# Kernel tuning notes

Hardware: AMD Instinct MI355X
Metric: run time of the kernel (lower is better)

The kernel has to match this reference:

```python
import jax, jax.numpy as jnp
import numpy as np

L, B, S, D, H, FF, V, P = 6, 8, 1024, 768, 12, 3072, 50257, 1024
DH = D // H
EPS = 1e-5


def setup_inputs() -> dict:
    key = jax.random.key(0)
    ks = jax.random.split(key, 12)
    std = 0.02
    return {
        "x_ids": jax.random.randint(ks[0], (B, S), 0, V),
        "calibrated_mask": jax.random.normal(ks[1], (B, S, S), jnp.float32),
        "wte": jax.random.normal(ks[2], (V, D), jnp.float32) * std,
        "wpe": jax.random.normal(ks[3], (P, D), jnp.float32) * std,
        "ln1_g": jnp.ones((L, D), jnp.float32),
        "ln1_b": jnp.zeros((L, D), jnp.float32),
        "qkv_w": jax.random.normal(ks[4], (L, D, 3 * D), jnp.float32) * std,
        "qkv_b": jnp.zeros((L, 3 * D), jnp.float32),
        "ao_w": jax.random.normal(ks[5], (L, D, D), jnp.float32) * std,
        "ao_b": jnp.zeros((L, D), jnp.float32),
        "ln2_g": jnp.ones((L, D), jnp.float32),
        "ln2_b": jnp.zeros((L, D), jnp.float32),
        "fc_w": jax.random.normal(ks[6], (L, D, FF), jnp.float32) * std,
        "fc_b": jnp.zeros((L, FF), jnp.float32),
        "op_w": jax.random.normal(ks[7], (L, FF, D), jnp.float32) * std,
        "op_b": jnp.zeros((L, D), jnp.float32),
        "lnf_g": jnp.ones((D,), jnp.float32),
        "lnf_b": jnp.zeros((D,), jnp.float32),
    }


def _ln(x, g, b):
    m = jnp.mean(x, axis=-1, keepdims=True)
    v = jnp.var(x, axis=-1, keepdims=True)
    return (x - m) * jax.lax.rsqrt(v + EPS) * g + b


def _gelu_new(x):
    c = np.sqrt(2.0 / np.pi).astype(np.float32)
    return 0.5 * x * (1.0 + jnp.tanh(c * (x + 0.044715 * x * x * x)))


def _gpt2_forward(x_ids, calibrated_mask, wte, wpe, ln1_g, ln1_b, qkv_w, qkv_b,
                  ao_w, ao_b, ln2_g, ln2_b, fc_w, fc_b, op_w, op_b, lnf_g, lnf_b):
    s = x_ids.shape[1]
    h = wte[x_ids] + wpe[:s][None, :, :]  # [B,S,D]
    causal = jnp.tril(jnp.ones((s, s), bool))
    neg = jnp.finfo(h.dtype).min
    # additive mask, broadcast over heads (unsqueeze(1).repeat over n_head)
    add_mask = calibrated_mask[:, None, :, :]  # [B,1,S,S]

    def block(hid, p):
        l1g, l1b, qw, qb, aw, ab, l2g, l2b, fw, fb, ow, ob = p
        x = _ln(hid, l1g, l1b)
        qkv = x @ qw + qb  # [B,S,3D]
        q, k, v = jnp.split(qkv, 3, axis=-1)
        q = q.reshape(q.shape[0], s, H, DH).transpose(0, 2, 1, 3)
        k = k.reshape(k.shape[0], s, H, DH).transpose(0, 2, 1, 3)
        v = v.reshape(v.shape[0], s, H, DH).transpose(0, 2, 1, 3)
        scores = jnp.einsum('bhqd,bhkd->bhqk', q, k) / jnp.sqrt(jnp.asarray(DH, q.dtype))
        scores = jnp.where(causal[None, None], scores, neg)
        scores = scores + add_mask
        w = jax.nn.softmax(scores, axis=-1)
        a = jnp.einsum('bhqk,bhkd->bhqd', w, v)
        a = a.transpose(0, 2, 1, 3).reshape(a.shape[0], s, D)
        hid = hid + a @ aw + ab
        x2 = _ln(hid, l2g, l2b)
        hid = hid + _gelu_new(x2 @ fw + fb) @ ow + ob
        return hid, None

    params = (ln1_g, ln1_b, qkv_w, qkv_b, ao_w, ao_b, ln2_g, ln2_b, fc_w, fc_b, op_w, op_b)
    h, _ = jax.lax.scan(block, h, params)
    return _ln(h, lnf_g, lnf_b)


def reference(x_ids, calibrated_mask, wte, wpe, ln1_g, ln1_b, qkv_w, qkv_b,
              ao_w, ao_b, ln2_g, ln2_b, fc_w, fc_b, op_w, op_b, lnf_g, lnf_b):
    return _gpt2_forward(x_ids, calibrated_mask, wte, wpe, ln1_g, ln1_b, qkv_w, qkv_b,
                         ao_w, ao_b, ln2_g, ln2_b, fc_w, fc_b, op_w, op_b, lnf_g, lnf_b)
```

## Files before the change

### kernel.cpp

```cpp
#include <hip/hip_runtime.h>
#include <hip/hip_bf16.h>

typedef __bf16 bf16_t;
typedef __bf16 bf16x8 __attribute__((ext_vector_type(8)));
typedef float  f32x4  __attribute__((ext_vector_type(4)));

#define DEV __device__ __forceinline__

DEV void gload_lds16(const void* g, void* l) {
  __builtin_amdgcn_global_load_lds(
      (__attribute__((address_space(1))) void*)(void*)g,
      (__attribute__((address_space(3))) void*)l, 16, 0, 0);
}

__global__ __launch_bounds__(256)
void transpose_cast(const float* __restrict__ in, bf16_t* __restrict__ out,
                    int K, int N) {
  __shared__ float tile[32][33];
  const int k0 = blockIdx.x * 32;
  const int n0 = blockIdx.y * 32;
  const int tx = threadIdx.x;
  const int ty = threadIdx.y;
#pragma unroll
  for (int i = 0; i < 32; i += 8)
    tile[ty + i][tx] = in[(long)(k0 + ty + i) * N + n0 + tx];
  __syncthreads();
#pragma unroll
  for (int i = 0; i < 32; i += 8)
    out[(long)(n0 + ty + i) * K + k0 + tx] = (bf16_t)tile[tx][ty + i];
}

__global__ __launch_bounds__(256)
void embed_kernel(const int* __restrict__ ids, const float* __restrict__ wte,
                  const float* __restrict__ wpe, float* __restrict__ h) {
  const int idx = blockIdx.x * 256 + threadIdx.x;
  const int col = idx % 768;
  const int row = idx / 768;
  const int s   = row & 1023;
  h[idx] = wte[(long)ids[row] * 768 + col] + wpe[s * 768 + col];
}

template <bool BF16OUT>
__global__ __launch_bounds__(256)
void ln_kernel(const float* __restrict__ x, const float* __restrict__ g,
               const float* __restrict__ b, bf16_t* __restrict__ ob,
               float* __restrict__ of) {
  const long row = blockIdx.x;
  const float* xr = x + row * 768;
  const int t = threadIdx.x;
  float v0 = xr[t], v1 = xr[t + 256], v2 = xr[t + 512];
  float s  = v0 + v1 + v2;
  float sq = v0 * v0 + v1 * v1 + v2 * v2;
#pragma unroll
  for (int o = 32; o; o >>= 1) { s += __shfl_down(s, o); sq += __shfl_down(sq, o); }
  __shared__ float red[8];
  const int w = t >> 6;
  if ((t & 63) == 0) { red[w] = s; red[4 + w] = sq; }
  __syncthreads();
  s  = red[0] + red[1] + red[2] + red[3];
  sq = red[4] + red[5] + red[6] + red[7];
  const float mean = s * (1.f / 768.f);
  const float rs = rsqrtf(sq * (1.f / 768.f) - mean * mean + 1e-5f);
  float vv[3] = {v0, v1, v2};
#pragma unroll
  for (int i = 0; i < 3; ++i) {
    const int col = t + i * 256;
    const float o2 = (vv[i] - mean) * rs * g[col] + b[col];
    if (BF16OUT) ob[row * 768 + col] = (bf16_t)o2;
    else         of[row * 768 + col] = o2;
  }
}

template <int EPI, int BN>
__global__ __launch_bounds__(256)
void gemm_bt(const bf16_t* __restrict__ A, const bf16_t* __restrict__ Bt,
             const float* __restrict__ bias, float* __restrict__ Cf,
             bf16_t* __restrict__ Cb, int M, int N, int K) {
  constexpr int NI = BN / 32;
  __shared__ bf16_t As[2][128 * 64];
  __shared__ bf16_t Bs[2][BN * 64];
  const int tid  = threadIdx.x;
  const int lane = tid & 63, w = tid >> 6;
  const int col = lane & 15, s16 = lane >> 4;
  const int nbn = N / BN;
  const int cpx = gridDim.x >> 3;
  const int bid = (blockIdx.x & 7) * cpx + (blockIdx.x >> 3);
  const int bm = bid / nbn, bn = bid % nbn;
  const int wr = w >> 1, wc = w & 1;

  f32x4 acc[4][NI];
#pragma unroll
  for (int i = 0; i < 4; ++i)
#pragma unroll
    for (int j = 0; j < NI; ++j) acc[i][j] = f32x4{0.f, 0.f, 0.f, 0.f};

  const long arow0 = (long)bm * 128;
  const long brow0 = (long)bn * BN;

  auto stage = [&](int buf, int k0) {
#pragma unroll
    for (int i = 0; i < 4; ++i) {
      const int c = i * 256 + tid;
      const int row = c >> 3, slot = c & 7;
      gload_lds16(A + (arow0 + row) * (long)K + k0 + ((slot ^ (row & 7)) << 3),
                  (char*)&As[buf][0] + i * 4096 + w * 1024);
    }
#pragma unroll
    for (int i = 0; i < BN / 32; ++i) {
      const int c = i * 256 + tid;
      const int row = c >> 3, slot = c & 7;
      gload_lds16(Bt + (brow0 + row) * (long)K + k0 + ((slot ^ (row & 7)) << 3),
                  (char*)&Bs[buf][0] + i * 4096 + w * 1024);
    }
  };

  const int nt = K >> 6;
  stage(0, 0);
  __syncthreads();
  int cur = 0;

  for (int t = 0; t < nt; ++t) {
    if (t + 1 < nt) stage(cur ^ 1, (t + 1) << 6);

    bf16x8 af[2][4], bfr[2][NI];
#pragma unroll
    for (int mi = 0; mi < 4; ++mi) {
      const int row = wr * 64 + mi * 16 + col;
#pragma unroll
      for (int ks = 0; ks < 2; ++ks) {
        const int slot = ks * 4 + s16;
        af[ks][mi] = *(const bf16x8*)((char*)&As[cur][0] + row * 128 +
                                      ((slot ^ (row & 7)) << 4));
      }
    }
#pragma unroll
    for (int ni = 0; ni < NI; ++ni) {
      const int row = wc * (BN / 2) + ni * 16 + col;
#pragma unroll
      for (int ks = 0; ks < 2; ++ks) {
        const int slot = ks * 4 + s16;
        bfr[ks][ni] = *(const bf16x8*)((char*)&Bs[cur][0] + row * 128 +
                                       ((slot ^ (row & 7)) << 4));
      }
    }
#pragma unroll
    for (int ks = 0; ks < 2; ++ks)
#pragma unroll
      for (int mi = 0; mi < 4; ++mi)
#pragma unroll
        for (int ni = 0; ni < NI; ++ni)
          acc[mi][ni] = __builtin_amdgcn_mfma_f32_16x16x32_bf16(
              af[ks][mi], bfr[ks][ni], acc[mi][ni], 0, 0, 0);

    __syncthreads();
    cur ^= 1;
  }

  const int colb = bn * BN + wc * (BN / 2) + col;
  const int rowb = bm * 128 + wr * 64 + (s16 << 2);
#pragma unroll
  for (int ni = 0; ni < NI; ++ni) {
    const int ccol = colb + ni * 16;
    const float bv = bias[ccol];
#pragma unroll
    for (int mi = 0; mi < 4; ++mi) {
      const int row = rowb + mi * 16;
#pragma unroll
      for (int r = 0; r < 4; ++r) {
        const float v = acc[mi][ni][r] + bv;
        const long idx = (long)(row + r) * N + ccol;
        if (EPI == 0)      Cf[idx] = v;
        else if (EPI == 1) Cf[idx] += v;
        else if (EPI == 2) Cb[idx] = (bf16_t)v;
        else {
          const float z = 0.7978845608028654f * (v + 0.044715f * v * v * v);
          Cb[idx] = (bf16_t)(v / (1.f + __expf(-2.f * z)));
        }
      }
    }
  }
}

__global__ __launch_bounds__(256)
void attn_kernel(const bf16_t* __restrict__ qkv, const float* __restrict__ mask,
                 bf16_t* __restrict__ out) {
  __shared__ bf16_t Kl[64 * 64];
  __shared__ bf16_t Vt[64 * 64];
  __shared__ bf16_t Pl[4][16 * 64];
  const int tid = threadIdx.x, lane = tid & 63, w = tid >> 6;
  const int col = lane & 15, s16 = lane >> 4, l7 = lane & 7;
  const int qp = blockIdx.x & 7;
  const int bh = blockIdx.x >> 3;
  const int b = bh / 12, h = bh % 12;
  const int sw0 = (s16 ^ l7) << 4;
  const int sw1 = ((s16 + 4) ^ l7) << 4;
  char* const plw = (char*)&Pl[w][0];

#pragma unroll 1
  for (int pass = 0; pass < 2; ++pass) {
    const int qt = pass ? (15 - qp) : qp;
    const int qrow0 = qt * 64 + w * 16;
    const long rowQ = (long)(b * 1024 + qrow0 + col) * 2304 + h * 64;
    const bf16x8 aq0 = *(const bf16x8*)&qkv[rowQ + s16 * 8];
    const bf16x8 aq1 = *(const bf16x8*)&qkv[rowQ + 32 + s16 * 8];
    const int qb = qrow0 + s16 * 4;
    const float* mrow = mask + ((long)b * 1024 + qb) * 1024;

    float m_run[4], l_run[4];
    f32x4 o_acc[4];
#pragma unroll
    for (int r = 0; r < 4; ++r) { m_run[r] = -INFINITY; l_run[r] = 0.f; }
#pragma unroll
    for (int go = 0; go < 4; ++go) o_acc[go] = f32x4{0.f, 0.f, 0.f, 0.f};

#pragma unroll 1
    for (int kt = 0; kt <= qt; ++kt) {
      const int k0 = kt * 64;
#pragma unroll
      for (int i = 0; i < 2; ++i) {
        const int c = i * 256 + tid;
        const int krow = c >> 3, slot = c & 7;
        gload_lds16(qkv + (long)(b * 1024 + k0 + krow) * 2304 + 768 + h * 64 +
                        ((slot ^ (krow & 7)) << 3),
                    (char*)Kl + i * 4096 + w * 1024);
      }
#pragma unroll
      for (int i = 0; i < 2; ++i) {
        const int c = i * 256 + tid;
        const int d = c & 63, koct = c >> 6;
        const bf16_t* vsrc = qkv + (long)(b * 1024 + k0 + koct * 8) * 2304 + 1536 + h * 64 + d;
        bf16x8 tv;
#pragma unroll
        for (int j = 0; j < 8; ++j) tv[j] = vsrc[(long)j * 2304];
        *(bf16x8*)((char*)Vt + d * 128 + ((koct ^ (d & 7)) << 4)) = tv;
      }
      float msk[4][4];
#pragma unroll
      for (int g = 0; g < 4; ++g)
#pragma unroll
        for (int r = 0; r < 4; ++r)
          msk[g][r] = mrow[(long)r * 1024 + k0 + g * 16 + col];
      __syncthreads();

      f32x4 sf[4];
#pragma unroll
      for (int g = 0; g < 4; ++g) {
        const int rbyte = (g * 16 + col) * 128;
        bf16x8 bk0 = *(const bf16x8*)((char*)Kl + rbyte + sw0);
        bf16x8 bk1 = *(const bf16x8*)((char*)Kl + rbyte + sw1);
        f32x4 z = f32x4{0.f, 0.f, 0.f, 0.f};
        z = __builtin_amdgcn_mfma_f32_16x16x32_bf16(aq0, bk0, z, 0, 0, 0);
        z = __builtin_amdgcn_mfma_f32_16x16x32_bf16(aq1, bk1, z, 0, 0, 0);
        sf[g] = z;
      }

      const bool diag = (kt == qt);
      float sv[4][4];
#pragma unroll
      for (int g = 0; g < 4; ++g)
#pragma unroll
        for (int r = 0; r < 4; ++r) {
          float s = sf[g][r] * 0.125f + msk[g][r];
          if (diag && (k0 + g * 16 + col) > (qb + r)) s = -INFINITY;
          sv[g][r] = s;
        }
#pragma unroll
      for (int r = 0; r < 4; ++r) {
        float mx = fmaxf(fmaxf(sv[0][r], sv[1][r]), fmaxf(sv[2][r], sv[3][r]));
#pragma unroll
        for (int o = 8; o; o >>= 1) mx = fmaxf(mx, __shfl_xor(mx, o));
        const float m_new = fmaxf(m_run[r], mx);
        const float f = __expf(m_run[r] - m_new);
        m_run[r] = m_new;
        float sum = 0.f;
#pragma unroll
        for (int g = 0; g < 4; ++g) {
          const float p = __expf(sv[g][r] - m_new);
          sv[g][r] = p;
          sum += p;
        }
#pragma unroll
        for (int o = 8; o; o >>= 1) sum += __shfl_xor(sum, o);
        l_run[r] = l_run[r] * f + sum;
#pragma unroll
        for (int go = 0; go < 4; ++go) o_acc[go][r] *= f;
      }

#pragma unroll
      for (int g = 0; g < 4; ++g) {
        const int ks = 2 * g + (col >> 3);
#pragma unroll
        for (int r = 0; r < 4; ++r) {
          const int qr = s16 * 4 + r;
          *(bf16_t*)(plw + qr * 128 + ((ks ^ (qr & 7)) << 4) + l7 * 2) = (bf16_t)sv[g][r];
        }
      }
      const bf16x8 pa0 = *(const bf16x8*)(plw + col * 128 + sw0);
      const bf16x8 pa1 = *(const bf16x8*)(plw + col * 128 + sw1);
#pragma unroll
      for (int go = 0; go < 4; ++go) {
        const int dbyte = (go * 16 + col) * 128;
        bf16x8 bv0 = *(const bf16x8*)((char*)Vt + dbyte + sw0);
        bf16x8 bv1 = *(const bf16x8*)((char*)Vt + dbyte + sw1);
        o_acc[go] = __builtin_amdgcn_mfma_f32_16x16x32_bf16(pa0, bv0, o_acc[go], 0, 0, 0);
        o_acc[go] = __builtin_amdgcn_mfma_f32_16x16x32_bf16(pa1, bv1, o_acc[go], 0, 0, 0);
      }
      __syncthreads();
    }

    float inv[4];
#pragma unroll
    for (int r = 0; r < 4; ++r) inv[r] = 1.f / l_run[r];
#pragma unroll
    for (int go = 0; go < 4; ++go)
#pragma unroll
      for (int r = 0; r < 4; ++r)
        out[(long)(b * 1024 + qb + r) * 768 + h * 64 + go * 16 + col] =
            (bf16_t)(o_acc[go][r] * inv[r]);
  }
}

extern "C" void kernel_launch(void* const* d_in, const int* in_sizes, int n_in,
                              void* d_out, int out_size, void* d_ws, size_t ws_size,
                              hipStream_t stream) {
  const int*   x_ids = (const int*)d_in[0];
  const float* mask  = (const float*)d_in[1];
  const float* wte   = (const float*)d_in[2];
  const float* wpe   = (const float*)d_in[3];
  const float* ln1_g = (const float*)d_in[4];
  const float* ln1_b = (const float*)d_in[5];
  const float* qkv_w = (const float*)d_in[6];
  const float* qkv_b = (const float*)d_in[7];
  const float* ao_w  = (const float*)d_in[8];
  const float* ao_b  = (const float*)d_in[9];
  const float* ln2_g = (const float*)d_in[10];
  const float* ln2_b = (const float*)d_in[11];
  const float* fc_w  = (const float*)d_in[12];
  const float* fc_b  = (const float*)d_in[13];
  const float* op_w  = (const float*)d_in[14];
  const float* op_b  = (const float*)d_in[15];
  const float* lnf_g = (const float*)d_in[16];
  const float* lnf_b = (const float*)d_in[17];

  char* ws = (char*)d_ws;
  size_t off = 0;
  auto alloc = [&](size_t bytes) {
    char* p = ws + off;
    off += (bytes + 255) & ~(size_t)255;
    return p;
  };
  bf16_t* wqT = (bf16_t*)alloc(6ull * 2304 * 768 * 2);
  bf16_t* waT = (bf16_t*)alloc(6ull * 768 * 768 * 2);
  bf16_t* wfT = (bf16_t*)alloc(6ull * 3072 * 768 * 2);
  bf16_t* woT = (bf16_t*)alloc(6ull * 768 * 3072 * 2);
  float*  h   = (float*) alloc(8192ull * 768 * 4);
  bf16_t* xb  = (bf16_t*)alloc(8192ull * 768 * 2);
  bf16_t* qkv = (bf16_t*)alloc(8192ull * 2304 * 2);
  bf16_t* abf = (bf16_t*)alloc(8192ull * 768 * 2);
  bf16_t* fb  = (bf16_t*)alloc(8192ull * 3072 * 2);
  if (off > ws_size) return;

  const dim3 tb(32, 8);
  for (int l = 0; l < 6; ++l) {
    transpose_cast<<<dim3(768 / 32, 2304 / 32), tb, 0, stream>>>(
        qkv_w + (long)l * 768 * 2304, wqT + (long)l * 2304 * 768, 768, 2304);
    transpose_cast<<<dim3(768 / 32, 768 / 32), tb, 0, stream>>>(
        ao_w + (long)l * 768 * 768, waT + (long)l * 768 * 768, 768, 768);
    transpose_cast<<<dim3(768 / 32, 3072 / 32), tb, 0, stream>>>(
        fc_w + (long)l * 768 * 3072, wfT + (long)l * 3072 * 768, 768, 3072);
    transpose_cast<<<dim3(3072 / 32, 768 / 32), tb, 0, stream>>>(
        op_w + (long)l * 3072 * 768, woT + (long)l * 768 * 3072, 3072, 768);
  }

  embed_kernel<<<24576, 256, 0, stream>>>(x_ids, wte, wpe, h);

  for (int l = 0; l < 6; ++l) {
    ln_kernel<true><<<8192, 256, 0, stream>>>(h, ln1_g + l * 768, ln1_b + l * 768, xb, nullptr);
    gemm_bt<2, 128><<<64 * 18, 256, 0, stream>>>(xb, wqT + (long)l * 2304 * 768,
                                                 qkv_b + l * 2304, nullptr, qkv, 8192, 2304, 768);
    attn_kernel<<<768, 256, 0, stream>>>(qkv, mask, abf);
    gemm_bt<1, 64><<<64 * 12, 256, 0, stream>>>(abf, waT + (long)l * 768 * 768,
                                                ao_b + l * 768, h, nullptr, 8192, 768, 768);
    ln_kernel<true><<<8192, 256, 0, stream>>>(h, ln2_g + l * 768, ln2_b + l * 768, xb, nullptr);
    gemm_bt<3, 128><<<64 * 24, 256, 0, stream>>>(xb, wfT + (long)l * 3072 * 768,
                                                 fc_b + l * 3072, nullptr, fb, 8192, 3072, 768);
    gemm_bt<1, 64><<<64 * 12, 256, 0, stream>>>(fb, woT + (long)l * 768 * 3072,
                                                op_b + l * 768, h, nullptr, 8192, 768, 3072);
  }

  ln_kernel<false><<<8192, 256, 0, stream>>>(h, lnf_g, lnf_b, nullptr, (float*)d_out);
}
```

Before: 1.789 ms.

## Double-buffer K/V tiles and prefetch mask in attention kernel

The attention kernel now keeps two LDS buffers for K and transposed V. It issues the global loads for the next key tile (K via direct-to-LDS, V and mask into registers) before computing the current tile, so memory latency overlaps with the MFMA and softmax work and one barrier per iteration is removed. It also raises wave priority around the MFMA sections and adds an occupancy hint to launch bounds. The cost is double the K/V LDS footprint and more live registers for the prefetched V and mask, which could reduce occupancy.

```diff
diff --git a/kernel.cpp b/kernel.cpp
--- a/kernel.cpp
+++ b/kernel.cpp
@@ -181,11 +181,11 @@
   }
 }
 
-__global__ __launch_bounds__(256)
+__global__ __launch_bounds__(256, 3)
 void attn_kernel(const bf16_t* __restrict__ qkv, const float* __restrict__ mask,
                  bf16_t* __restrict__ out) {
-  __shared__ bf16_t Kl[64 * 64];
-  __shared__ bf16_t Vt[64 * 64];
+  __shared__ bf16_t Kl[2][64 * 64];
+  __shared__ bf16_t Vt[2][64 * 64];
   __shared__ bf16_t Pl[4][16 * 64];
   const int tid = threadIdx.x, lane = tid & 63, w = tid >> 6;
   const int col = lane & 15, s16 = lane >> 4, l7 = lane & 7;
@@ -195,6 +195,40 @@
   const int sw0 = (s16 ^ l7) << 4;
   const int sw1 = ((s16 + 4) ^ l7) << 4;
   char* const plw = (char*)&Pl[w][0];
+  const long qkvb = (long)b * 1024 * 2304;
+
+  auto stageK = [&](int buf, int k0) {
+#pragma unroll
+    for (int i = 0; i < 2; ++i) {
+      const int c = i * 256 + tid;
+      const int krow = c >> 3, slot = c & 7;
+      gload_lds16(qkv + qkvb + (long)(k0 + krow) * 2304 + 768 + h * 64 +
+                      ((slot ^ (krow & 7)) << 3),
+                  (char*)&Kl[buf][0] + i * 4096 + w * 1024);
+    }
+  };
+  auto loadV = [&](int k0, bf16x8& t0, bf16x8& t1) {
+    const bf16_t* vbase = qkv + qkvb + 1536 + h * 64;
+#pragma unroll
+    for (int i = 0; i < 2; ++i) {
+      const int c = i * 256 + tid;
+      const int d = c & 63, koct = c >> 6;
+      const bf16_t* vsrc = vbase + (long)(k0 + koct * 8) * 2304 + d;
+      bf16x8 tv;
+#pragma unroll
+      for (int j = 0; j < 8; ++j) tv[j] = vsrc[(long)j * 2304];
+      if (i == 0) t0 = tv; else t1 = tv;
+    }
+  };
+  auto storeV = [&](int buf, const bf16x8& t0, const bf16x8& t1) {
+#pragma unroll
+    for (int i = 0; i < 2; ++i) {
+      const int c = i * 256 + tid;
+      const int d = c & 63, koct = c >> 6;
+      *(bf16x8*)((char*)&Vt[buf][0] + d * 128 + ((koct ^ (d & 7)) << 4)) =
+          (i == 0) ? t0 : t1;
+    }
+  };
 
 #pragma unroll 1
   for (int pass = 0; pass < 2; ++pass) {
@@ -206,6 +240,14 @@
     const int qb = qrow0 + s16 * 4;
     const float* mrow = mask + ((long)b * 1024 + qb) * 1024;
 
+    auto loadM = [&](int k0, float (&m)[4][4]) {
+#pragma unroll
+      for (int g = 0; g < 4; ++g)
+#pragma unroll
+        for (int r = 0; r < 4; ++r)
+          m[g][r] = mrow[(long)r * 1024 + k0 + g * 16 + col];
+    };
+
     float m_run[4], l_run[4];
     f32x4 o_acc[4];
 #pragma unroll
@@ -213,46 +255,39 @@
 #pragma unroll
     for (int go = 0; go < 4; ++go) o_acc[go] = f32x4{0.f, 0.f, 0.f, 0.f};
 
+    bf16x8 tv0, tv1;
+    stageK(0, 0);
+    loadV(0, tv0, tv1);
+    storeV(0, tv0, tv1);
+    float msk[4][4];
+    loadM(0, msk);
+    __syncthreads();
+
 #pragma unroll 1
     for (int kt = 0; kt <= qt; ++kt) {
+      const int cur = kt & 1;
+      const bool more = kt < qt;
       const int k0 = kt * 64;
-#pragma unroll
-      for (int i = 0; i < 2; ++i) {
-        const int c = i * 256 + tid;
-        const int krow = c >> 3, slot = c & 7;
-        gload_lds16(qkv + (long)(b * 1024 + k0 + krow) * 2304 + 768 + h * 64 +
-                        ((slot ^ (krow & 7)) << 3),
-                    (char*)Kl + i * 4096 + w * 1024);
-      }
-#pragma unroll
-      for (int i = 0; i < 2; ++i) {
-        const int c = i * 256 + tid;
-        const int d = c & 63, koct = c >> 6;
-        const bf16_t* vsrc = qkv + (long)(b * 1024 + k0 + koct * 8) * 2304 + 1536 + h * 64 + d;
-        bf16x8 tv;
-#pragma unroll
-        for (int j = 0; j < 8; ++j) tv[j] = vsrc[(long)j * 2304];
-        *(bf16x8*)((char*)Vt + d * 128 + ((koct ^ (d & 7)) << 4)) = tv;
-      }
-      float msk[4][4];
-#pragma unroll
-      for (int g = 0; g < 4; ++g)
-#pragma unroll
-        for (int r = 0; r < 4; ++r)
-          msk[g][r] = mrow[(long)r * 1024 + k0 + g * 16 + col];
-      __syncthreads();
+      float mnx[4][4];
+      if (more) {
+        stageK(cur ^ 1, k0 + 64);
+        loadV(k0 + 64, tv0, tv1);
+        loadM(k0 + 64, mnx);
+      }
 
       f32x4 sf[4];
+      __builtin_amdgcn_s_setprio(1);
 #pragma unroll
       for (int g = 0; g < 4; ++g) {
         const int rbyte = (g * 16 + col) * 128;
-        bf16x8 bk0 = *(const bf16x8*)((char*)Kl + rbyte + sw0);
-        bf16x8 bk1 = *(const bf16x8*)((char*)Kl + rbyte + sw1);
+        bf16x8 bk0 = *(const bf16x8*)((char*)&Kl[cur][0] + rbyte + sw0);
+        bf16x8 bk1 = *(const bf16x8*)((char*)&Kl[cur][0] + rbyte + sw1);
         f32x4 z = f32x4{0.f, 0.f, 0.f, 0.f};
         z = __builtin_amdgcn_mfma_f32_16x16x32_bf16(aq0, bk0, z, 0, 0, 0);
         z = __builtin_amdgcn_mfma_f32_16x16x32_bf16(aq1, bk1, z, 0, 0, 0);
         sf[g] = z;
       }
+      __builtin_amdgcn_s_setprio(0);
 
       const bool diag = (kt == qt);
       float sv[4][4];
@@ -297,13 +332,23 @@
       }
       const bf16x8 pa0 = *(const bf16x8*)(plw + col * 128 + sw0);
       const bf16x8 pa1 = *(const bf16x8*)(plw + col * 128 + sw1);
+      __builtin_amdgcn_s_setprio(1);
 #pragma unroll
       for (int go = 0; go < 4; ++go) {
         const int dbyte = (go * 16 + col) * 128;
-        bf16x8 bv0 = *(const bf16x8*)((char*)Vt + dbyte + sw0);
-        bf16x8 bv1 = *(const bf16x8*)((char*)Vt + dbyte + sw1);
+        bf16x8 bv0 = *(const bf16x8*)((char*)&Vt[cur][0] + dbyte + sw0);
+        bf16x8 bv1 = *(const bf16x8*)((char*)&Vt[cur][0] + dbyte + sw1);
         o_acc[go] = __builtin_amdgcn_mfma_f32_16x16x32_bf16(pa0, bv0, o_acc[go], 0, 0, 0);
         o_acc[go] = __builtin_amdgcn_mfma_f32_16x16x32_bf16(pa1, bv1, o_acc[go], 0, 0, 0);
+      }
+      __builtin_amdgcn_s_setprio(0);
+
+      if (more) {
+        storeV(cur ^ 1, tv0, tv1);
+#pragma unroll
+        for (int g = 0; g < 4; ++g)
+#pragma unroll
+          for (int r = 0; r < 4; ++r) msk[g][r] = mnx[g][r];
       }
       __syncthreads();
     }
```

Result: no change. 1.769 ms (-1.1%).
